# Performance work log

Hardware: AMD Instinct MI355X
Metric: run time of the kernel (lower is better)

The kernel has to match this reference:

```python
import jax, jax.numpy as jnp
import numpy as np

# Neighbor offsets (di, dj) implied by each 3x3 kernel: out_j = gray - shift(gray, di, dj)
# kernel0..kernel7 as defined in the torch module (center weight +1, one neighbor -1)
OFFSETS = [(0, -1), (1, -1), (1, 0), (1, 1), (0, 1), (-1, 1), (-1, 0), (-1, -1)]
EPS = 1e-5  # torch InstanceNorm2d default


def setup_inputs() -> dict:
    key = jax.random.key(0)
    x = jax.random.uniform(key, (8, 3, 1024, 1024), dtype=jnp.float32)
    return {"x": x}


def _ltpe(x):
    # RGB -> gray, [B,1,H,W]
    g = (0.3 * x[:, 0] + 0.59 * x[:, 1] + 0.11 * x[:, 2])[:, None]
    B, _, H, W = g.shape
    gp = jnp.pad(g, ((0, 0), (0, 0), (1, 1), (1, 1)))  # zero pad = conv padding=1
    out = jnp.zeros_like(g)
    for j, (di, dj) in enumerate(OFFSETS):
        nb = gp[:, :, 1 + di:1 + di + H, 1 + dj:1 + dj + W]
        d = (g - nb + 1.0) * 0.5          # (conv_out + 1) * 0.5
        out = out + d * (float(2 ** j) / 255.0)
    # InstanceNorm2d(1): per (b, c) mean/biased-var over spatial dims, no affine
    mean = jnp.mean(out, axis=(2, 3), keepdims=True)
    var = jnp.var(out, axis=(2, 3), keepdims=True)
    out = (out - mean) * jax.lax.rsqrt(var + EPS)
    return jnp.concatenate([out, out, out], axis=1)  # [B,3,H,W]


def reference(x):
    return _ltpe(x)
```

## Files before the change

kernel.cpp:

```cpp
#include <hip/hip_runtime.h>
#include <math.h>

constexpr int H = 1024, W = 1024, B = 8;
constexpr int NPIX = H * W;
constexpr int ROWS = 2;
constexpr int RG   = H / ROWS;

__device__ __forceinline__ void gload_lds16(const float* g, float* l) {
    __builtin_amdgcn_global_load_lds(
        (const __attribute__((address_space(1))) void*)g,
        (__attribute__((address_space(3))) void*)l, 16, 0, 0);
}

__global__ __launch_bounds__(256)
void ltpe_stage1(const float* __restrict__ x, float* __restrict__ out,
                 float2* __restrict__ part)
{
    __shared__ float lds[4][3][W];
    const int b   = blockIdx.y;
    const int k   = blockIdx.x;
    const int kg  = ((k & 7) << 6) | (k >> 3);
    const int r0  = kg * ROWS;
    const int tid = threadIdx.x;
    const int w   = tid >> 6;
    const int l   = tid & 63;
    const int c   = tid << 2;
    const float* xb = x + (size_t)b * 3 * NPIX;

    #pragma unroll
    for (int s = 0; s < 4; ++s) {
        const int rr = r0 - 1 + s;
        if ((unsigned)rr < (unsigned)H) {
            #pragma unroll
            for (int ch = 0; ch < 3; ++ch) {
                const float* gp = xb + (size_t)ch * NPIX + (size_t)rr * W + (w << 8) + (l << 2);
                gload_lds16(gp, &lds[s][ch][w << 8]);
            }
        } else {
            const float4 z = make_float4(0.f, 0.f, 0.f, 0.f);
            #pragma unroll
            for (int ch = 0; ch < 3; ++ch)
                *reinterpret_cast<float4*>(&lds[s][ch][c]) = z;
        }
    }
    __syncthreads();

    const int ql = (tid == 0)   ? 0   : tid - 1;
    const int qr = (tid == 255) ? 255 : tid + 1;
    float g6[4][6];
    #pragma unroll
    for (int s = 0; s < 4; ++s) {
        const float4 o0 = *reinterpret_cast<const float4*>(&lds[s][0][c]);
        const float4 o1 = *reinterpret_cast<const float4*>(&lds[s][1][c]);
        const float4 o2 = *reinterpret_cast<const float4*>(&lds[s][2][c]);
        const float4 l0 = *reinterpret_cast<const float4*>(&lds[s][0][ql << 2]);
        const float4 l1 = *reinterpret_cast<const float4*>(&lds[s][1][ql << 2]);
        const float4 l2 = *reinterpret_cast<const float4*>(&lds[s][2][ql << 2]);
        const float4 rq0 = *reinterpret_cast<const float4*>(&lds[s][0][qr << 2]);
        const float4 rq1 = *reinterpret_cast<const float4*>(&lds[s][1][qr << 2]);
        const float4 rq2 = *reinterpret_cast<const float4*>(&lds[s][2][qr << 2]);
        g6[s][1] = 0.3f * o0.x + 0.59f * o1.x + 0.11f * o2.x;
        g6[s][2] = 0.3f * o0.y + 0.59f * o1.y + 0.11f * o2.y;
        g6[s][3] = 0.3f * o0.z + 0.59f * o1.z + 0.11f * o2.z;
        g6[s][4] = 0.3f * o0.w + 0.59f * o1.w + 0.11f * o2.w;
        g6[s][0] = (tid == 0)   ? 0.f : 0.3f * l0.w  + 0.59f * l1.w  + 0.11f * l2.w;
        g6[s][5] = (tid == 255) ? 0.f : 0.3f * rq0.x + 0.59f * rq1.x + 0.11f * rq2.x;
    }

    constexpr float w0 = 1.f/255.f,  w1 = 2.f/255.f,  w2 = 4.f/255.f,  w3 = 8.f/255.f,
                    w4 = 16.f/255.f, w5 = 32.f/255.f, w6 = 64.f/255.f, w7 = 128.f/255.f;
    float s = 0.f, ss = 0.f;
    float* ob = out + (size_t)b * 3 * NPIX + (size_t)r0 * W + c;
    #pragma unroll
    for (int rr = 0; rr < ROWS; ++rr) {
        const float (&up)[6] = g6[rr];
        const float (&mi)[6] = g6[rr + 1];
        const float (&dn)[6] = g6[rr + 2];
        float tv[4];
        #pragma unroll
        for (int kk = 0; kk < 4; ++kk) {
            float sv = w0 * mi[kk];
            sv = fmaf(w1, dn[kk],     sv);
            sv = fmaf(w2, dn[kk + 1], sv);
            sv = fmaf(w3, dn[kk + 2], sv);
            sv = fmaf(w4, mi[kk + 2], sv);
            sv = fmaf(w5, up[kk + 2], sv);
            sv = fmaf(w6, up[kk + 1], sv);
            sv = fmaf(w7, up[kk],     sv);
            tv[kk] = 0.5f * mi[kk + 1] + 0.5f - 0.5f * sv;
            s += tv[kk];
            ss = fmaf(tv[kk], tv[kk], ss);
        }
        float4 t4 = {tv[0], tv[1], tv[2], tv[3]};
        *reinterpret_cast<float4*>(ob + (size_t)rr * W) = t4;
    }

    #pragma unroll
    for (int off = 32; off >= 1; off >>= 1) {
        s  += __shfl_down(s, off);
        ss += __shfl_down(ss, off);
    }
    __shared__ float2 wred[4];
    if (l == 0) wred[w] = make_float2(s, ss);
    __syncthreads();
    if (tid == 0) {
        float2 a0 = wred[0], a1 = wred[1], a2 = wred[2], a3 = wred[3];
        part[(size_t)b * RG + kg] = make_float2(a0.x + a1.x + a2.x + a3.x,
                                                a0.y + a1.y + a2.y + a3.y);
    }
}

__global__ __launch_bounds__(256)
void ltpe_stageB(float* __restrict__ out, const float2* __restrict__ part)
{
    const int b    = blockIdx.y;
    const int r    = blockIdx.x;
    const int tid  = threadIdx.x;
    const int lane = tid & 63;

    const float4* pp = reinterpret_cast<const float4*>(part + (size_t)b * RG);
    const float4 u = pp[tid];
    double s  = (double)u.x + (double)u.z;
    double ss = (double)u.y + (double)u.w;
    #pragma unroll
    for (int off = 32; off >= 1; off >>= 1) {
        s  += __shfl_down(s, off);
        ss += __shfl_down(ss, off);
    }
    __shared__ double red[8];
    __shared__ float2 mv;
    const int wv = tid >> 6;
    if (lane == 0) { red[wv] = s; red[4 + wv] = ss; }
    __syncthreads();
    if (tid == 0) {
        const double S  = red[0] + red[1] + red[2] + red[3];
        const double SS = red[4] + red[5] + red[6] + red[7];
        const double n    = (double)NPIX;
        const double mean = S / n;
        const double var  = SS / n - mean * mean;
        mv = make_float2((float)mean, (float)(1.0 / sqrt(var + 1e-5)));
    }
    __syncthreads();
    const float mean = mv.x, rstd = mv.y;

    const size_t base = (size_t)b * 3 * NPIX + (size_t)r * W + (tid << 2);
    const float4 t4 = *reinterpret_cast<const float4*>(out + base);
    float4 y;
    y.x = (t4.x - mean) * rstd;
    y.y = (t4.y - mean) * rstd;
    y.z = (t4.z - mean) * rstd;
    y.w = (t4.w - mean) * rstd;
    *reinterpret_cast<float4*>(out + base)            = y;
    *reinterpret_cast<float4*>(out + base + NPIX)     = y;
    *reinterpret_cast<float4*>(out + base + 2 * NPIX) = y;
}

extern "C" void kernel_launch(void* const* d_in, const int* in_sizes, int n_in,
                              void* d_out, int out_size, void* d_ws, size_t ws_size,
                              hipStream_t stream)
{
    const float* x = (const float*)d_in[0];
    float* out = (float*)d_out;
    float2* part = (float2*)d_ws;

    ltpe_stage1<<<dim3(RG, B), 256, 0, stream>>>(x, out, part);
    ltpe_stageB<<<dim3(H, B), 256, 0, stream>>>(out, part);
}
```

Measured before the change: 51.65 us.

## Fuse gray/LTP and instance-norm into one cooperative kernel with grid sync

```diff
diff --git a/kernel.cpp b/kernel.cpp
--- a/kernel.cpp
+++ b/kernel.cpp
@@ -1,8 +1,134 @@
 #include <hip/hip_runtime.h>
+#include <hip/hip_cooperative_groups.h>
 #include <math.h>
+
+namespace cg = cooperative_groups;
 
 constexpr int H = 1024, W = 1024, B = 8;
 constexpr int NPIX = H * W;
+
+constexpr int FROWS = 8;
+constexpr int FGRID = B * (H / FROWS);
+
+__device__ __forceinline__ float grayat(const float* __restrict__ xb, int r, int c) {
+    const float* p = xb + (size_t)r * W + c;
+    return 0.3f * p[0] + 0.59f * p[NPIX] + 0.11f * p[2 * NPIX];
+}
+
+__global__ __launch_bounds__(256, 4)
+void ltpe_fused(const float* __restrict__ x, float* __restrict__ out,
+                float2* __restrict__ part)
+{
+    const int blk  = blockIdx.x;
+    const int b    = blk & 7;
+    const int g    = blk >> 3;
+    const int r0   = g * FROWS;
+    const int tid  = threadIdx.x;
+    const int c    = tid << 2;
+    const int lane = tid & 63;
+    const float* xb = x + (size_t)b * 3 * NPIX;
+
+    constexpr float w0 = 1.f/255.f,  w1 = 2.f/255.f,  w2 = 4.f/255.f,  w3 = 8.f/255.f,
+                    w4 = 16.f/255.f, w5 = 32.f/255.f, w6 = 64.f/255.f, w7 = 128.f/255.f;
+
+    auto grayrow = [&](int rr, float (&dst)[6]) {
+        float4 q0 = {0.f,0.f,0.f,0.f}, q1 = q0, q2 = q0;
+        const bool rok = (unsigned)rr < (unsigned)H;
+        if (rok) {
+            const float* p = xb + (size_t)rr * W + c;
+            q0 = *reinterpret_cast<const float4*>(p);
+            q1 = *reinterpret_cast<const float4*>(p + NPIX);
+            q2 = *reinterpret_cast<const float4*>(p + 2 * NPIX);
+        }
+        float4 gq;
+        gq.x = 0.3f * q0.x + 0.59f * q1.x + 0.11f * q2.x;
+        gq.y = 0.3f * q0.y + 0.59f * q1.y + 0.11f * q2.y;
+        gq.z = 0.3f * q0.z + 0.59f * q1.z + 0.11f * q2.z;
+        gq.w = 0.3f * q0.w + 0.59f * q1.w + 0.11f * q2.w;
+        float l  = __shfl_up(gq.w, 1);
+        float rt = __shfl_down(gq.x, 1);
+        if (lane == 0)  l  = (c > 0 && rok)     ? grayat(xb, rr, c - 1) : 0.f;
+        if (lane == 63) rt = (c + 4 < W && rok) ? grayat(xb, rr, c + 4) : 0.f;
+        dst[0] = l; dst[1] = gq.x; dst[2] = gq.y; dst[3] = gq.z; dst[4] = gq.w; dst[5] = rt;
+    };
+
+    float gray[3][6];
+    float4 tq[FROWS];
+    float s = 0.f, ss = 0.f;
+
+    #pragma unroll
+    for (int i = 0; i < FROWS + 2; ++i) {
+        grayrow(r0 - 1 + i, gray[i % 3]);
+        if (i >= 2) {
+            const float (&up)[6] = gray[(i - 2) % 3];
+            const float (&mi)[6] = gray[(i - 1) % 3];
+            const float (&dn)[6] = gray[i % 3];
+            float tv[4];
+            #pragma unroll
+            for (int kk = 0; kk < 4; ++kk) {
+                float sv = w0 * mi[kk];
+                sv = fmaf(w1, dn[kk],     sv);
+                sv = fmaf(w2, dn[kk + 1], sv);
+                sv = fmaf(w3, dn[kk + 2], sv);
+                sv = fmaf(w4, mi[kk + 2], sv);
+                sv = fmaf(w5, up[kk + 2], sv);
+                sv = fmaf(w6, up[kk + 1], sv);
+                sv = fmaf(w7, up[kk],     sv);
+                tv[kk] = 0.5f * mi[kk + 1] + 0.5f - 0.5f * sv;
+                s += tv[kk];
+                ss = fmaf(tv[kk], tv[kk], ss);
+            }
+            tq[i - 2] = make_float4(tv[0], tv[1], tv[2], tv[3]);
+        }
+    }
+
+    #pragma unroll
+    for (int off = 32; off >= 1; off >>= 1) {
+        s  += __shfl_down(s, off);
+        ss += __shfl_down(ss, off);
+    }
+    __shared__ float2 wred[4];
+    if (lane == 0) wred[tid >> 6] = make_float2(s, ss);
+    __syncthreads();
+    if (tid == 0) {
+        float2 a0 = wred[0], a1 = wred[1], a2 = wred[2], a3 = wred[3];
+        part[(size_t)b * 128 + g] = make_float2(a0.x + a1.x + a2.x + a3.x,
+                                                a0.y + a1.y + a2.y + a3.y);
+    }
+
+    cg::this_grid().sync();
+
+    const float4* pp = reinterpret_cast<const float4*>(part + (size_t)b * 128);
+    const float4 u = pp[lane];
+    double ds = (double)u.x + (double)u.z;
+    double dss = (double)u.y + (double)u.w;
+    #pragma unroll
+    for (int off = 1; off <= 32; off <<= 1) {
+        ds  += __shfl_xor(ds, off);
+        dss += __shfl_xor(dss, off);
+    }
+    const double n    = (double)NPIX;
+    const double dmean = ds / n;
+    const double dvar  = dss / n - dmean * dmean;
+    const float mean = (float)dmean;
+    const float rstd = (float)(1.0 / sqrt(dvar + 1e-5));
+
+    float* ob = out + (size_t)b * 3 * NPIX + (size_t)r0 * W + c;
+    #pragma unroll
+    for (int rr = 0; rr < FROWS; ++rr) {
+        const float4 t4 = tq[rr];
+        float4 y;
+        y.x = (t4.x - mean) * rstd;
+        y.y = (t4.y - mean) * rstd;
+        y.z = (t4.z - mean) * rstd;
+        y.w = (t4.w - mean) * rstd;
+        float* p = ob + (size_t)rr * W;
+        *reinterpret_cast<float4*>(p)            = y;
+        *reinterpret_cast<float4*>(p + NPIX)     = y;
+        *reinterpret_cast<float4*>(p + 2 * NPIX) = y;
+    }
+}
+
 constexpr int ROWS = 2;
 constexpr int RG   = H / ROWS;
 
@@ -163,6 +289,16 @@
     float* out = (float*)d_out;
     float2* part = (float2*)d_ws;
 
-    ltpe_stage1<<<dim3(RG, B), 256, 0, stream>>>(x, out, part);
-    ltpe_stageB<<<dim3(H, B), 256, 0, stream>>>(out, part);
-}
+    int nb = 0;
+    hipError_t qe = hipOccupancyMaxActiveBlocksPerMultiprocessor(
+        &nb, reinterpret_cast<const void*>(ltpe_fused), 256, 0);
+
+    if (qe == hipSuccess && nb * 256 >= FGRID) {
+        void* args[] = { (void*)&x, (void*)&out, (void*)&part };
+        hipLaunchCooperativeKernel((void*)ltpe_fused, dim3(FGRID), dim3(256),
+                                   args, 0, stream);
+    } else {
+        ltpe_stage1<<<dim3(RG, B), 256, 0, stream>>>(x, out, part);
+        ltpe_stageB<<<dim3(H, B), 256, 0, stream>>>(out, part);
+    }
+}
```

Measured after the change: 51.15 us. Within noise of the previous version (-1.0%).
